# Performance work log

Measured on AMD Instinct MI355X. Metric: run time of the kernel, lower is better.

Reference implementation:

```python
import jax, jax.numpy as jnp
import numpy as np

B, S, D, H, HD = 4, 2048, 1024, 16, 64
MLP = 4 * D
ROPE_BASE = 10000.0
TARGET_SPARSITY = 0.2


def _rotate_half(t):
    return jnp.concatenate([-t[..., HD // 2:], t[..., :HD // 2]], axis=-1)


def setup_inputs() -> dict:
    key = jax.random.key(0)
    ks = jax.random.split(key, 10)
    s = 0.02
    return {
        "x": jax.random.normal(ks[0], (B, S, D), jnp.float32),
        "gate_w": jax.random.normal(ks[1], (D, 1), jnp.float32) * s,
        "gate_b": jnp.zeros((1,), jnp.float32),
        "wq": jax.random.normal(ks[2], (D, D), jnp.float32) * s,
        "wk": jax.random.normal(ks[3], (D, D), jnp.float32) * s,
        "wv": jax.random.normal(ks[4], (D, D), jnp.float32) * s,
        "wo": jax.random.normal(ks[5], (D, D), jnp.float32) * s,
        "conv_w": jax.random.normal(ks[6], (D, 3), jnp.float32) * s,  # depthwise k=3
        "conv_b": jnp.zeros((D,), jnp.float32),
        "mlp_w1": jax.random.normal(ks[7], (D, MLP), jnp.float32) * s,
        "mlp_b1": jnp.zeros((MLP,), jnp.float32),
        "mlp_w2": jax.random.normal(ks[8], (MLP, D), jnp.float32) * s,
        "mlp_b2": jnp.zeros((D,), jnp.float32),
    }


def reference(x, gate_w, gate_b, wq, wk, wv, wo, conv_w, conv_b,
              mlp_w1, mlp_b1, mlp_w2, mlp_b2):
    # --- Router (eval path: hard threshold, mask_ste == active mask) ---
    logits = x @ gate_w + gate_b                    # [B,S,1]
    probs = jax.nn.sigmoid(logits)
    aux_loss = (probs.mean() - TARGET_SPARSITY) ** 2
    mask = (probs > 0.5).astype(x.dtype)            # [B,S,1]

    # --- Reflexive stream: causal depthwise conv (left pad 2) + MLP ---
    xp = jnp.pad(x, ((0, 0), (2, 0), (0, 0)))       # [B,S+2,D]
    x_conv = (xp[:, 0:S] * conv_w[:, 0]
              + xp[:, 1:S + 1] * conv_w[:, 1]
              + xp[:, 2:S + 2] * conv_w[:, 2] + conv_b)
    shallow = jax.nn.relu(x_conv @ mlp_w1 + mlp_b1) @ mlp_w2 + mlp_b2

    # --- Contextual stream: RoPE causal attention, queries gated by router ---
    q = (x @ wq).reshape(B, S, H, HD)
    k = (x @ wk).reshape(B, S, H, HD)
    v = (x @ wv).reshape(B, S, H, HD)

    pos = jnp.arange(S)
    inv_freq = 1.0 / (ROPE_BASE ** (jnp.arange(0, HD, 2, dtype=jnp.float32) / HD))
    freqs = pos[:, None].astype(jnp.float32) * inv_freq[None, :]
    emb = jnp.concatenate([freqs, freqs], axis=-1)  # [S,HD]
    cos = jnp.cos(emb)[None, :, None, :]
    sin = jnp.sin(emb)[None, :, None, :]
    q = q * cos + _rotate_half(q) * sin
    k = k * cos + _rotate_half(k) * sin

    scale = 1.0 / np.sqrt(HD)
    scores = jnp.einsum('bqhd,bkhd->bhqk', q, k) * scale
    causal = pos[:, None] >= pos[None, :]           # [S,S]
    scores = jnp.where(causal[None, None], scores, jnp.finfo(scores.dtype).min)
    attn = jax.nn.softmax(scores, axis=-1)
    ctx = jnp.einsum('bhqk,bkhd->bqhd', attn, v).reshape(B, S, D)
    ctx = (ctx @ wo) * mask                         # scatter back: only active queries contribute

    out = x + shallow + ctx
    return out, aux_loss
```

## Files before the change

### kernel.cpp

```cpp
#include <hip/hip_runtime.h>
#include <hip/hip_bf16.h>

#define DDIM 1024
#define SLEN 2048
#define NTOK 8192
#define MLPD 4096

typedef float f32x4 __attribute__((ext_vector_type(4)));
typedef __bf16 bf16x8 __attribute__((ext_vector_type(8)));

__device__ __forceinline__ void async16(void* lds, const void* g) {
  __builtin_amdgcn_global_load_lds(
      (__attribute__((address_space(1))) void*)g,
      (__attribute__((address_space(3))) void*)lds, 16, 0, 0);
}

template <int N> struct VMC { static constexpr int v = N; };

__global__ __launch_bounds__(256) void prep_kernel(
    const float* __restrict__ x, const float* __restrict__ gate_w,
    const float* __restrict__ gate_b, const float* __restrict__ conv_w,
    const float* __restrict__ conv_b, __bf16* __restrict__ xb,
    __bf16* __restrict__ xcb, float* __restrict__ maskp,
    float* __restrict__ probsp) {
  const int tok = blockIdx.x, t = threadIdx.x;
  const int s = tok & (SLEN - 1);
  const float* xr = x + (size_t)tok * DDIM;
  float4 v = ((const float4*)xr)[t];
  float4 g = ((const float4*)gate_w)[t];
  float part = v.x * g.x + v.y * g.y + v.z * g.z + v.w * g.w;
#pragma unroll
  for (int d = 32; d; d >>= 1) part += __shfl_down(part, d);
  __shared__ float ws4[4];
  const int lane = t & 63, w = t >> 6;
  if (lane == 0) ws4[w] = part;
  __syncthreads();
  if (t == 0) {
    float logit = ws4[0] + ws4[1] + ws4[2] + ws4[3] + gate_b[0];
    float prob = 1.f / (1.f + __expf(-logit));
    probsp[tok] = prob;
    maskp[tok] = prob > 0.5f ? 1.f : 0.f;
  }
  union { ushort4 u; __bf16 b[4]; } xo;
  xo.b[0] = (__bf16)v.x; xo.b[1] = (__bf16)v.y;
  xo.b[2] = (__bf16)v.z; xo.b[3] = (__bf16)v.w;
  ((ushort4*)(xb + (size_t)tok * DDIM))[t] = xo.u;
  float4 zero4 = {0.f, 0.f, 0.f, 0.f};
  float4 m1 = (s >= 1) ? ((const float4*)(xr - DDIM))[t] : zero4;
  float4 m2 = (s >= 2) ? ((const float4*)(xr - 2 * DDIM))[t] : zero4;
  int d0 = t * 4;
  float vv[4] = {v.x, v.y, v.z, v.w};
  float a1[4] = {m1.x, m1.y, m1.z, m1.w};
  float a2[4] = {m2.x, m2.y, m2.z, m2.w};
  union { ushort4 u; __bf16 b[4]; } co;
#pragma unroll
  for (int i = 0; i < 4; ++i) {
    float c0 = conv_w[(d0 + i) * 3 + 0];
    float c1 = conv_w[(d0 + i) * 3 + 1];
    float c2 = conv_w[(d0 + i) * 3 + 2];
    float r = a2[i] * c0 + a1[i] * c1 + vv[i] * c2 + conv_b[d0 + i];
    co.b[i] = (__bf16)r;
  }
  ((ushort4*)(xcb + (size_t)tok * DDIM))[t] = co.u;
}

__global__ __launch_bounds__(256) void tabgen_kernel(float2* __restrict__ tab) {
  const int idx = blockIdx.x * 256 + threadIdx.x;
  const int s = idx >> 5, i = idx & 31;
  float invf = __builtin_amdgcn_exp2f(-(float)i * (13.28771238f / 32.f));
  float fr = (float)s * invf;
  tab[idx] = make_float2(cosf(fr), sinf(fr));
}

__global__ __launch_bounds__(256) void tcast_kernel(const float* __restrict__ src,
                                                    __bf16* __restrict__ dst,
                                                    int K, int N) {
  __shared__ __bf16 tile[64][65];
  const int n0 = blockIdx.x * 64, k0 = blockIdx.y * 64;
  const int t = threadIdx.x;
  const int cr = (t & 15) * 4;
#pragma unroll
  for (int i = 0; i < 4; ++i) {
    int rr = (t >> 4) + i * 16;
    float4 v = *(const float4*)(src + (size_t)(k0 + rr) * N + n0 + cr);
    tile[rr][cr + 0] = (__bf16)v.x; tile[rr][cr + 1] = (__bf16)v.y;
    tile[rr][cr + 2] = (__bf16)v.z; tile[rr][cr + 3] = (__bf16)v.w;
  }
  __syncthreads();
#pragma unroll
  for (int i = 0; i < 2; ++i) {
    int c = t + i * 256;
    int nl = c >> 3, koff = (c & 7) * 8;
    union { uint4 u; __bf16 b[8]; } o;
#pragma unroll
    for (int j = 0; j < 8; ++j) o.b[j] = tile[koff + j][nl];
    *(uint4*)(dst + (size_t)(n0 + nl) * K + k0 + koff) = o.u;
  }
}

template <int EPI, bool ROPE>
__global__ __launch_bounds__(512, 2) void gemm256p(
    const __bf16* __restrict__ A, const __bf16* __restrict__ Bt,
    const float* __restrict__ bias, const float2* __restrict__ tab,
    __bf16* __restrict__ Cb, int M, int N, int K) {
  extern __shared__ char sm[];
  const int t = threadIdx.x, lane = t & 63, w = t >> 6;
  const int c = lane & 15, g = lane >> 4;
  const int nwg = gridDim.x * gridDim.y;
  const int wgid = blockIdx.y * gridDim.x + blockIdx.x;
  const int swz = (wgid & 7) * (nwg >> 3) + (wgid >> 3);
  const int m0 = (swz / gridDim.x) * 256, n0 = (swz % gridDim.x) * 256;
  const int wm = (w >> 2) * 128, wn = (w & 3) * 64;

  f32x4 acc[8][4] = {};
  const int nk = K >> 5;

  auto stage = [&](int buf, int kt) {
    const int k0 = kt << 5;
    char* base = sm + buf * 32768;
#pragma unroll
    for (int r = 0; r < 2; ++r) {
      int o = ((r * 8 + w) << 10) + (lane << 4);
      int rp = o >> 7;
      int u = (o >> 4) & 7;
      int l = u ^ (rp & 7);
      int mr = rp * 2 + (l >> 2);
      int kk = (l & 3) * 8;
      async16(base + o, A + (size_t)(m0 + mr) * K + k0 + kk);
      async16(base + 16384 + o, Bt + (size_t)(n0 + mr) * K + k0 + kk);
    }
  };

  auto body = [&](auto vmc, int tt, bool dostage) {
    if (dostage) stage((tt + 3) & 3, tt + 3);
    asm volatile("s_waitcnt vmcnt(%0)" ::"n"(decltype(vmc)::v) : "memory");
    __builtin_amdgcn_s_barrier();
    asm volatile("" ::: "memory");
    const char* Ab = sm + (tt & 3) * 32768;
    const char* Bb = Ab + 16384;
    bf16x8 aq[8], bq[4];
#pragma unroll
    for (int nt = 0; nt < 4; ++nt) {
      int row = wn + nt * 16 + c;
      int rp = row >> 1;
      int u = ((row & 1) * 4 + g) ^ (rp & 7);
      bq[nt] = *(const bf16x8*)(Bb + rp * 128 + u * 16);
    }
#pragma unroll
    for (int i = 0; i < 8; ++i) {
      int row = wm + i * 16 + c;
      int rp = row >> 1;
      int u = ((row & 1) * 4 + g) ^ (rp & 7);
      aq[i] = *(const bf16x8*)(Ab + rp * 128 + u * 16);
    }
    __builtin_amdgcn_s_setprio(1);
#pragma unroll
    for (int i = 0; i < 8; ++i)
#pragma unroll
      for (int nt = 0; nt < 4; ++nt)
        acc[i][nt] = __builtin_amdgcn_mfma_f32_16x16x32_bf16(
            aq[i], bq[nt], acc[i][nt], 0, 0, 0);
    __builtin_amdgcn_s_setprio(0);
    __builtin_amdgcn_s_barrier();
    asm volatile("" ::: "memory");
  };

  stage(0, 0);
  stage(1, 1);
  stage(2, 2);
  int tt = 0;
  for (; tt < nk - 3; ++tt) body(VMC<12>{}, tt, true);
  body(VMC<8>{}, tt, false); ++tt;
  body(VMC<4>{}, tt, false); ++tt;
  body(VMC<0>{}, tt, false);

  if (ROPE && n0 < 2048) {
#pragma unroll
    for (int i = 0; i < 8; ++i)
#pragma unroll
      for (int r = 0; r < 4; ++r) {
        int s = (m0 + wm + i * 16 + g * 4 + r) & (SLEN - 1);
        float2 t0 = tab[s * 32 + c];
        float2 t1 = tab[s * 32 + 16 + c];
        float q0 = acc[i][0][r], q2 = acc[i][2][r];
        acc[i][0][r] = q0 * t0.x - q2 * t0.y;
        acc[i][2][r] = q2 * t0.x + q0 * t0.y;
        float q1 = acc[i][1][r], q3 = acc[i][3][r];
        acc[i][1][r] = q1 * t1.x - q3 * t1.y;
        acc[i][3][r] = q3 * t1.x + q1 * t1.y;
      }
  }

#pragma unroll
  for (int i = 0; i < 8; ++i)
#pragma unroll
    for (int nt = 0; nt < 4; ++nt)
#pragma unroll
      for (int r = 0; r < 4; ++r) {
        int row = m0 + wm + i * 16 + g * 4 + r;
        int col = n0 + wn + nt * 16 + c;
        float v = acc[i][nt][r];
        size_t idx = (size_t)row * N + col;
        if constexpr (EPI == 0) {
          Cb[idx] = (__bf16)v;
        } else {
          v += bias[col];
          Cb[idx] = (__bf16)fmaxf(v, 0.f);
        }
      }
}

template <int EPI>
__global__ __launch_bounds__(256, 3) void gemm_bt(
    const __bf16* __restrict__ A, const __bf16* __restrict__ Bt,
    const float* __restrict__ bias, const float* __restrict__ xres,
    const float* __restrict__ maskp, __bf16* __restrict__ Cb,
    float* __restrict__ Cf, int M, int N, int K) {
  __shared__ char smem[32768];
  char* As = smem;
  char* Bs = smem + 16384;
  const int t = threadIdx.x, lane = t & 63, w = t >> 6;
  const int nwg = gridDim.x * gridDim.y;
  const int wgid = blockIdx.y * gridDim.x + blockIdx.x;
  const int swz = (wgid & 7) * (nwg >> 3) + (wgid >> 3);
  const int m0 = (swz / gridDim.x) * 128, n0 = (swz % gridDim.x) * 128;
  const int wm = (w >> 1) * 64, wn = (w & 1) * 64;
  f32x4 acc[4][4] = {};
  const int nk = K >> 6;
  for (int kt = 0; kt < nk; ++kt) {
    const int k0 = kt << 6;
#pragma unroll
    for (int rd = 0; rd < 4; ++rd) {
      int o = ((rd * 4 + w) << 10) + (lane << 4);
      int row = o >> 7;
      int us = ((o >> 4) & 7) ^ (row & 7);
      async16(As + o, A + (size_t)(m0 + row) * K + k0 + us * 8);
      async16(Bs + o, Bt + (size_t)(n0 + row) * K + k0 + us * 8);
    }
    __syncthreads();
#pragma unroll
    for (int ks = 0; ks < 2; ++ks) {
      bf16x8 af[4], bfr[4];
#pragma unroll
      for (int mt = 0; mt < 4; ++mt) {
        int row = wm + mt * 16 + (lane & 15);
        int u = (ks * 4 + (lane >> 4)) ^ (row & 7);
        af[mt] = *(const bf16x8*)(As + row * 128 + u * 16);
      }
#pragma unroll
      for (int nt = 0; nt < 4; ++nt) {
        int row = wn + nt * 16 + (lane & 15);
        int u = (ks * 4 + (lane >> 4)) ^ (row & 7);
        bfr[nt] = *(const bf16x8*)(Bs + row * 128 + u * 16);
      }
#pragma unroll
      for (int mt = 0; mt < 4; ++mt)
#pragma unroll
        for (int nt = 0; nt < 4; ++nt)
          acc[mt][nt] = __builtin_amdgcn_mfma_f32_16x16x32_bf16(
              af[mt], bfr[nt], acc[mt][nt], 0, 0, 0);
    }
    __syncthreads();
  }
#pragma unroll
  for (int mt = 0; mt < 4; ++mt)
#pragma unroll
    for (int nt = 0; nt < 4; ++nt)
#pragma unroll
      for (int r = 0; r < 4; ++r) {
        int row = m0 + wm + mt * 16 + ((lane >> 4) << 2) + r;
        int col = n0 + wn + nt * 16 + (lane & 15);
        float v = acc[mt][nt][r];
        size_t idx = (size_t)row * N + col;
        if constexpr (EPI == 2) {
          Cf[idx] = xres[idx] + v + bias[col];
        } else {
          Cf[idx] += maskp[row] * v;
        }
      }
}

__device__ __forceinline__ void scatterV(char* Vdst, int w, int lane,
                                         float4 va, float4 vb) {
  union { float4 f; __bf16 bv[8]; } u0, u1;
  u0.f = va; u1.f = vb;
#pragma unroll
  for (int j = 0; j < 8; ++j) {
    int d = w * 8 + j;
    int by = d * 128 + (((lane >> 3) ^ (d & 7)) << 4) + ((lane & 7) << 1);
    *(__bf16*)(Vdst + by) = u0.bv[j];
    int d2 = d + 32;
    int by2 = d2 * 128 + (((lane >> 3) ^ (d2 & 7)) << 4) + ((lane & 7) << 1);
    *(__bf16*)(Vdst + by2) = u1.bv[j];
  }
}

__global__ __launch_bounds__(256, 3) void attn_kernel(const __bf16* __restrict__ qkv,
                                                      __bf16* __restrict__ ctx) {
  __shared__ char sm[32768];
  const int t = threadIdx.x, lane = t & 63, w = t >> 6;
  const int c = lane & 15, g = lane >> 4, g4 = g * 4;
  const int bh = (int)blockIdx.x * 8 + ((int)blockIdx.y & 7);
  const int qp = (int)blockIdx.y >> 3;
  const int h = bh & 15, b = bh >> 4;
  const size_t tokbase = (size_t)b * SLEN;
  const __bf16* qg = qkv + tokbase * 3072 + h * 64;
  const __bf16* kg = qg + 1024;
  const __bf16* vg = qg + 2048;
  const float SCL = 0.125f * 1.44269504f;
  char* Ps = sm + (w << 12);
  char* Ks = sm + 16384;
  char* Vs = sm + 24576;

  for (int ph = 0; ph < 2; ++ph) {
    const int qt = ph == 0 ? qp : 15 - qp;
    const int q0 = qt * 128;
#pragma unroll
    for (int rd = 0; rd < 4; ++rd) {
      int o = ((rd * 4 + w) << 10) + (lane << 4);
      int row = o >> 7;
      int us = ((o >> 4) & 7) ^ (row & 7);
      async16(sm + o, qg + (size_t)(q0 + row) * 3072 + us * 8);
    }
    __syncthreads();
    bf16x8 qb[2][2];
#pragma unroll
    for (int mt = 0; mt < 2; ++mt)
#pragma unroll
      for (int ks = 0; ks < 2; ++ks) {
        int row = w * 32 + mt * 16 + c;
        int u = (ks * 4 + g) ^ (row & 7);
        qb[mt][ks] = *(const bf16x8*)(sm + row * 128 + u * 16);
      }

    float m_run[2] = {-1e30f, -1e30f}, l_run[2] = {0.f, 0.f};
    f32x4 o_acc[2][4] = {};
    const int nkt = (q0 + 128) >> 6;
    const int wrow0 = q0 + w * 32;

    for (int kt = 0; kt < nkt; ++kt) {
      const int k0 = kt << 6;
#pragma unroll
      for (int rd = 0; rd < 2; ++rd) {
        int o = ((rd * 4 + w) << 10) + (lane << 4);
        int row = o >> 7;
        int us = ((o >> 4) & 7) ^ (row & 7);
        async16(Ks + o, kg + (size_t)(k0 + row) * 3072 + us * 8);
      }
      {
        float4 va = *(const float4*)(vg + (size_t)(k0 + lane) * 3072 + w * 8);
        float4 vb2 = *(const float4*)(vg + (size_t)(k0 + lane) * 3072 + w * 8 + 32);
        scatterV(Vs, w, lane, va, vb2);
      }
      __syncthreads();
      if (k0 <= wrow0 + 31) {
        f32x4 st[4][2] = {};
        __builtin_amdgcn_s_setprio(1);
#pragma unroll
        for (int ks = 0; ks < 2; ++ks) {
          bf16x8 ka[4];
#pragma unroll
          for (int nt = 0; nt < 4; ++nt) {
            int row = nt * 16 + c;
            int u = (ks * 4 + g) ^ (row & 7);
            ka[nt] = *(const bf16x8*)(Ks + row * 128 + u * 16);
          }
#pragma unroll
          for (int nt = 0; nt < 4; ++nt)
#pragma unroll
            for (int mt = 0; mt < 2; ++mt)
              st[nt][mt] = __builtin_amdgcn_mfma_f32_16x16x32_bf16(
                  ka[nt], qb[mt][ks], st[nt][mt], 0, 0, 0);
        }
        __builtin_amdgcn_s_setprio(0);
        const bool needmask = (k0 + 63) > wrow0;
#pragma unroll
        for (int mt = 0; mt < 2; ++mt) {
          float mx = -1e30f;
          if (needmask) {
            int qglob = wrow0 + mt * 16 + c;
#pragma unroll
            for (int nt = 0; nt < 4; ++nt)
#pragma unroll
              for (int r = 0; r < 4; ++r) {
                float sv = st[nt][mt][r] * SCL;
                if (k0 + nt * 16 + g4 + r > qglob) sv = -1e30f;
                st[nt][mt][r] = sv;
                mx = fmaxf(mx, sv);
              }
          } else {
#pragma unroll
            for (int nt = 0; nt < 4; ++nt)
#pragma unroll
              for (int r = 0; r < 4; ++r) {
                float sv = st[nt][mt][r] * SCL;
                st[nt][mt][r] = sv;
                mx = fmaxf(mx, sv);
              }
          }
          mx = fmaxf(mx, __shfl_xor(mx, 16));
          mx = fmaxf(mx, __shfl_xor(mx, 32));
          const bool skip = __all(mx - m_run[mt] <= 8.f) != 0;
          float mnew = skip ? m_run[mt] : fmaxf(m_run[mt], mx);
          float rs = 0.f;
#pragma unroll
          for (int nt = 0; nt < 4; ++nt)
#pragma unroll
            for (int r = 0; r < 4; ++r) {
              float p = __builtin_amdgcn_exp2f(st[nt][mt][r] - mnew);
              st[nt][mt][r] = p;
              rs += p;
            }
          rs += __shfl_xor(rs, 16);
          rs += __shfl_xor(rs, 32);
          if (skip) {
            l_run[mt] += rs;
          } else {
            float fac = __builtin_amdgcn_exp2f(m_run[mt] - mnew);
            m_run[mt] = mnew;
            l_run[mt] = l_run[mt] * fac + rs;
#pragma unroll
            for (int r = 0; r < 4; ++r) {
              float fr = __shfl(fac, g * 20 + r);
#pragma unroll
              for (int dt = 0; dt < 4; ++dt) o_acc[mt][dt][r] *= fr;
            }
          }
          int rowq = mt * 16 + c;
          int rbase = rowq * 128 + 8 * (g & 1);
#pragma unroll
          for (int nt = 0; nt < 4; ++nt) {
            int us = (2 * nt + (g >> 1)) ^ (c & 7);
            union { uint2 v; __bf16 bb[4]; } pp;
            pp.bb[0] = (__bf16)st[nt][mt][0]; pp.bb[1] = (__bf16)st[nt][mt][1];
            pp.bb[2] = (__bf16)st[nt][mt][2]; pp.bb[3] = (__bf16)st[nt][mt][3];
            *(uint2*)(Ps + rbase + us * 16) = pp.v;
          }
        }
        __builtin_amdgcn_s_setprio(1);
#pragma unroll
        for (int ks = 0; ks < 2; ++ks) {
          bf16x8 pa[2], vb[4];
#pragma unroll
          for (int mt = 0; mt < 2; ++mt) {
            int row = mt * 16 + c;
            int u = (ks * 4 + g) ^ (row & 7);
            pa[mt] = *(const bf16x8*)(Ps + row * 128 + u * 16);
          }
#pragma unroll
          for (int dt = 0; dt < 4; ++dt) {
            int row = dt * 16 + c;
            int u = (ks * 4 + g) ^ (row & 7);
            vb[dt] = *(const bf16x8*)(Vs + row * 128 + u * 16);
          }
#pragma unroll
          for (int mt = 0; mt < 2; ++mt)
#pragma unroll
            for (int dt = 0; dt < 4; ++dt)
              o_acc[mt][dt] = __builtin_amdgcn_mfma_f32_16x16x32_bf16(
                  pa[mt], vb[dt], o_acc[mt][dt], 0, 0, 0);
        }
        __builtin_amdgcn_s_setprio(0);
      }
      __syncthreads();
    }
#pragma unroll
    for (int mt = 0; mt < 2; ++mt)
#pragma unroll
      for (int r = 0; r < 4; ++r) {
        float lr = __shfl(l_run[mt], g * 20 + r);
        float inv = 1.f / lr;
        int tokr = q0 + w * 32 + mt * 16 + g4 + r;
#pragma unroll
        for (int dt = 0; dt < 4; ++dt) {
          int d = dt * 16 + c;
          ctx[(tokbase + tokr) * DDIM + h * 64 + d] =
              (__bf16)(o_acc[mt][dt][r] * inv);
        }
      }
  }
}

__global__ __launch_bounds__(256) void aux_kernel(const float* __restrict__ probsp,
                                                  float* __restrict__ outp) {
  const int t = threadIdx.x;
  float sum = 0.f;
  for (int i = t; i < NTOK; i += 256) sum += probsp[i];
#pragma unroll
  for (int d = 32; d; d >>= 1) sum += __shfl_down(sum, d);
  __shared__ float ws4[4];
  if ((t & 63) == 0) ws4[t >> 6] = sum;
  __syncthreads();
  if (t == 0) {
    float m = (ws4[0] + ws4[1] + ws4[2] + ws4[3]) * (1.f / NTOK) - 0.2f;
    outp[0] = m * m;
  }
}

extern "C" void kernel_launch(void* const* d_in, const int* in_sizes, int n_in,
                              void* d_out, int out_size, void* d_ws, size_t ws_size,
                              hipStream_t stream) {
  const float* x      = (const float*)d_in[0];
  const float* gate_w = (const float*)d_in[1];
  const float* gate_b = (const float*)d_in[2];
  const float* wq     = (const float*)d_in[3];
  const float* wk     = (const float*)d_in[4];
  const float* wv     = (const float*)d_in[5];
  const float* wo     = (const float*)d_in[6];
  const float* conv_w = (const float*)d_in[7];
  const float* conv_b = (const float*)d_in[8];
  const float* mlp_w1 = (const float*)d_in[9];
  const float* mlp_b1 = (const float*)d_in[10];
  const float* mlp_w2 = (const float*)d_in[11];
  const float* mlp_b2 = (const float*)d_in[12];
  float* out = (float*)d_out;

  char* ws = (char*)d_ws;
  const size_t MB = 1ull << 20;
  __bf16* xb     = (__bf16*)(ws + 0);
  __bf16* xcb    = (__bf16*)(ws + 16 * MB);
  __bf16* ctx    = (__bf16*)(ws + 16 * MB);
  __bf16* wqkv_t = (__bf16*)(ws + 32 * MB);
  __bf16* wo_t   = (__bf16*)(ws + 38 * MB);
  __bf16* w1_t   = (__bf16*)(ws + 40 * MB);
  __bf16* w2_t   = (__bf16*)(ws + 48 * MB);
  float*  maskp  = (float*)(ws + 56 * MB);
  float*  probsp = (float*)(ws + 56 * MB + 65536);
  float2* ropetab= (float2*)(ws + 56 * MB + 131072);
  __bf16* h1     = (__bf16*)(ws + 57 * MB);
  __bf16* qkv    = (__bf16*)(ws + 57 * MB);

  prep_kernel<<<NTOK, 256, 0, stream>>>(x, gate_w, gate_b, conv_w, conv_b,
                                        xb, xcb, maskp, probsp);
  tabgen_kernel<<<256, 256, 0, stream>>>(ropetab);
  tcast_kernel<<<dim3(16, 16), 256, 0, stream>>>(wq, wqkv_t, 1024, 1024);
  tcast_kernel<<<dim3(16, 16), 256, 0, stream>>>(wk, wqkv_t + 1024 * 1024, 1024, 1024);
  tcast_kernel<<<dim3(16, 16), 256, 0, stream>>>(wv, wqkv_t + 2048 * 1024, 1024, 1024);
  tcast_kernel<<<dim3(16, 16), 256, 0, stream>>>(wo, wo_t, 1024, 1024);
  tcast_kernel<<<dim3(64, 16), 256, 0, stream>>>(mlp_w1, w1_t, 1024, 4096);
  tcast_kernel<<<dim3(16, 64), 256, 0, stream>>>(mlp_w2, w2_t, 4096, 1024);

  gemm256p<1, false><<<dim3(16, 32), 512, 131072, stream>>>(
      xcb, w1_t, mlp_b1, nullptr, h1, NTOK, MLPD, DDIM);
  gemm_bt<2><<<dim3(8, 64), 256, 0, stream>>>(h1, w2_t, mlp_b2, x, nullptr,
                                              nullptr, out, NTOK, DDIM, MLPD);
  gemm256p<0, true><<<dim3(12, 32), 512, 131072, stream>>>(
      xb, wqkv_t, nullptr, ropetab, qkv, NTOK, 3072, DDIM);
  attn_kernel<<<dim3(8, 64), 256, 0, stream>>>(qkv, ctx);
  gemm_bt<3><<<dim3(8, 64), 256, 0, stream>>>(ctx, wo_t, nullptr, nullptr, maskp,
                                              nullptr, out, NTOK, DDIM, DDIM);
  aux_kernel<<<1, 256, 0, stream>>>(probsp, out + (size_t)(out_size - 1));
}
```

Measured before the change: 393.4 us.

## Compact router-active queries and skip inactive tokens in attention and Wo GEMM

Adds a compaction kernel that builds a per-batch list of tokens whose router mask is active. Attention loads only those query rows through the index list, limits each tile's key range to the largest active position, and writes compacted context. The Wo GEMM skips row tiles beyond the active count and scatter-adds results to the original token rows, which removes the mask multiply. This cuts attention and output-projection work in proportion to sparsity. In exchange it adds a serial scan kernel, gather indirection, and load imbalance across attention blocks.

```diff
diff --git a/kernel.cpp b/kernel.cpp
--- a/kernel.cpp
+++ b/kernel.cpp
@@ -62,6 +62,35 @@
     co.b[i] = (__bf16)r;
   }
   ((ushort4*)(xcb + (size_t)tok * DDIM))[t] = co.u;
+}
+
+__global__ __launch_bounds__(256) void compact_kernel(
+    const float* __restrict__ maskp, int* __restrict__ act,
+    int* __restrict__ nact) {
+  const int b = blockIdx.x, t = threadIdx.x;
+  __shared__ int sc[256];
+  __shared__ int base;
+  if (t == 0) base = 0;
+  __syncthreads();
+  for (int ch = 0; ch < 8; ++ch) {
+    int tok = ch * 256 + t;
+    int m = maskp[b * 2048 + tok] > 0.5f ? 1 : 0;
+    sc[t] = m;
+    __syncthreads();
+#pragma unroll
+    for (int off = 1; off < 256; off <<= 1) {
+      int v = t >= off ? sc[t - off] : 0;
+      __syncthreads();
+      sc[t] += v;
+      __syncthreads();
+    }
+    if (m) act[b * 2048 + base + sc[t] - 1] = tok;
+    int tot = sc[255];
+    __syncthreads();
+    if (t == 0) base += tot;
+    __syncthreads();
+  }
+  if (t == 0) nact[b] = base;
 }
 
 __global__ __launch_bounds__(256) void tabgen_kernel(float2* __restrict__ tab) {
@@ -210,11 +239,9 @@
       }
 }
 
-template <int EPI>
-__global__ __launch_bounds__(256, 3) void gemm_bt(
+__global__ __launch_bounds__(256, 3) void gemm_bt2(
     const __bf16* __restrict__ A, const __bf16* __restrict__ Bt,
     const float* __restrict__ bias, const float* __restrict__ xres,
-    const float* __restrict__ maskp, __bf16* __restrict__ Cb,
     float* __restrict__ Cf, int M, int N, int K) {
   __shared__ char smem[32768];
   char* As = smem;
@@ -270,12 +297,76 @@
       for (int r = 0; r < 4; ++r) {
         int row = m0 + wm + mt * 16 + ((lane >> 4) << 2) + r;
         int col = n0 + wn + nt * 16 + (lane & 15);
-        float v = acc[mt][nt][r];
         size_t idx = (size_t)row * N + col;
-        if constexpr (EPI == 2) {
-          Cf[idx] = xres[idx] + v + bias[col];
-        } else {
-          Cf[idx] += maskp[row] * v;
+        Cf[idx] = xres[idx] + acc[mt][nt][r] + bias[col];
+      }
+}
+
+__global__ __launch_bounds__(256, 3) void gemm_wo(
+    const __bf16* __restrict__ A, const __bf16* __restrict__ Bt,
+    const int* __restrict__ act, const int* __restrict__ nact,
+    float* __restrict__ Cf, int M, int N, int K) {
+  __shared__ char smem[32768];
+  char* As = smem;
+  char* Bs = smem + 16384;
+  const int t = threadIdx.x, lane = t & 63, w = t >> 6;
+  const int nwg = gridDim.x * gridDim.y;
+  const int wgid = blockIdx.y * gridDim.x + blockIdx.x;
+  const int swz = (wgid & 7) * (nwg >> 3) + (wgid >> 3);
+  const int m0 = (swz / gridDim.x) * 128, n0 = (swz % gridDim.x) * 128;
+  const int b = m0 >> 11;
+  const int na = nact[b];
+  if ((m0 & 2047) >= na) return;
+  const int wm = (w >> 1) * 64, wn = (w & 1) * 64;
+  f32x4 acc[4][4] = {};
+  const int nk = K >> 6;
+  for (int kt = 0; kt < nk; ++kt) {
+    const int k0 = kt << 6;
+#pragma unroll
+    for (int rd = 0; rd < 4; ++rd) {
+      int o = ((rd * 4 + w) << 10) + (lane << 4);
+      int row = o >> 7;
+      int us = ((o >> 4) & 7) ^ (row & 7);
+      async16(As + o, A + (size_t)(m0 + row) * K + k0 + us * 8);
+      async16(Bs + o, Bt + (size_t)(n0 + row) * K + k0 + us * 8);
+    }
+    __syncthreads();
+#pragma unroll
+    for (int ks = 0; ks < 2; ++ks) {
+      bf16x8 af[4], bfr[4];
+#pragma unroll
+      for (int mt = 0; mt < 4; ++mt) {
+        int row = wm + mt * 16 + (lane & 15);
+        int u = (ks * 4 + (lane >> 4)) ^ (row & 7);
+        af[mt] = *(const bf16x8*)(As + row * 128 + u * 16);
+      }
+#pragma unroll
+      for (int nt = 0; nt < 4; ++nt) {
+        int row = wn + nt * 16 + (lane & 15);
+        int u = (ks * 4 + (lane >> 4)) ^ (row & 7);
+        bfr[nt] = *(const bf16x8*)(Bs + row * 128 + u * 16);
+      }
+#pragma unroll
+      for (int mt = 0; mt < 4; ++mt)
+#pragma unroll
+        for (int nt = 0; nt < 4; ++nt)
+          acc[mt][nt] = __builtin_amdgcn_mfma_f32_16x16x32_bf16(
+              af[mt], bfr[nt], acc[mt][nt], 0, 0, 0);
+    }
+    __syncthreads();
+  }
+#pragma unroll
+  for (int mt = 0; mt < 4; ++mt)
+#pragma unroll
+    for (int nt = 0; nt < 4; ++nt)
+#pragma unroll
+      for (int r = 0; r < 4; ++r) {
+        int row = m0 + wm + mt * 16 + ((lane >> 4) << 2) + r;
+        int col = n0 + wn + nt * 16 + (lane & 15);
+        int jj = row & 2047;
+        if (jj < na) {
+          int tok = act[b * 2048 + jj];
+          Cf[((size_t)b * 2048 + tok) * N + col] += acc[mt][nt][r];
         }
       }
 }
@@ -295,14 +386,19 @@
   }
 }
 
-__global__ __launch_bounds__(256, 3) void attn_kernel(const __bf16* __restrict__ qkv,
-                                                      __bf16* __restrict__ ctx) {
+__global__ __launch_bounds__(256, 3) void attn_kernel(
+    const __bf16* __restrict__ qkv, __bf16* __restrict__ ctx,
+    const int* __restrict__ act, const int* __restrict__ nact) {
   __shared__ char sm[32768];
   const int t = threadIdx.x, lane = t & 63, w = t >> 6;
   const int c = lane & 15, g = lane >> 4, g4 = g * 4;
-  const int bh = (int)blockIdx.x * 8 + ((int)blockIdx.y & 7);
-  const int qp = (int)blockIdx.y >> 3;
+  const int bh = (int)blockIdx.x;
   const int h = bh & 15, b = bh >> 4;
+  const int na = nact[b];
+  const int ntile = (na + 127) >> 7;
+  const int j = 15 - (int)blockIdx.y;
+  if (j >= ntile) return;
+  const int* actb = act + b * 2048;
   const size_t tokbase = (size_t)b * SLEN;
   const __bf16* qg = qkv + tokbase * 3072 + h * 64;
   const __bf16* kg = qg + 1024;
@@ -312,173 +408,180 @@
   char* Ks = sm + 16384;
   char* Vs = sm + 24576;
 
-  for (int ph = 0; ph < 2; ++ph) {
-    const int qt = ph == 0 ? qp : 15 - qp;
-    const int q0 = qt * 128;
-#pragma unroll
-    for (int rd = 0; rd < 4; ++rd) {
+  const int q0 = j * 128;
+#pragma unroll
+  for (int rd = 0; rd < 4; ++rd) {
+    int o = ((rd * 4 + w) << 10) + (lane << 4);
+    int row = o >> 7;
+    int us = ((o >> 4) & 7) ^ (row & 7);
+    int cr = q0 + row; if (cr > na - 1) cr = na - 1;
+    async16(sm + o, qg + (size_t)actb[cr] * 3072 + us * 8);
+  }
+  __syncthreads();
+  bf16x8 qb[2][2];
+#pragma unroll
+  for (int mt = 0; mt < 2; ++mt)
+#pragma unroll
+    for (int ks = 0; ks < 2; ++ks) {
+      int row = w * 32 + mt * 16 + c;
+      int u = (ks * 4 + g) ^ (row & 7);
+      qb[mt][ks] = *(const bf16x8*)(sm + row * 128 + u * 16);
+    }
+  int qpos[2];
+#pragma unroll
+  for (int mt = 0; mt < 2; ++mt) {
+    int rr = q0 + w * 32 + mt * 16 + c; if (rr > na - 1) rr = na - 1;
+    qpos[mt] = actb[rr];
+  }
+  int rf = q0 + w * 32;       if (rf > na - 1) rf = na - 1;
+  int rl = q0 + w * 32 + 31;  if (rl > na - 1) rl = na - 1;
+  const int wmin = actb[rf], wmax = actb[rl];
+  int bl = q0 + 127;          if (bl > na - 1) bl = na - 1;
+  const int nkt = (actb[bl] >> 6) + 1;
+
+  float m_run[2] = {-1e30f, -1e30f}, l_run[2] = {0.f, 0.f};
+  f32x4 o_acc[2][4] = {};
+
+  for (int kt = 0; kt < nkt; ++kt) {
+    const int k0 = kt << 6;
+#pragma unroll
+    for (int rd = 0; rd < 2; ++rd) {
       int o = ((rd * 4 + w) << 10) + (lane << 4);
       int row = o >> 7;
       int us = ((o >> 4) & 7) ^ (row & 7);
-      async16(sm + o, qg + (size_t)(q0 + row) * 3072 + us * 8);
-    }
-    __syncthreads();
-    bf16x8 qb[2][2];
-#pragma unroll
-    for (int mt = 0; mt < 2; ++mt)
+      async16(Ks + o, kg + (size_t)(k0 + row) * 3072 + us * 8);
+    }
+    {
+      float4 va = *(const float4*)(vg + (size_t)(k0 + lane) * 3072 + w * 8);
+      float4 vb2 = *(const float4*)(vg + (size_t)(k0 + lane) * 3072 + w * 8 + 32);
+      scatterV(Vs, w, lane, va, vb2);
+    }
+    __syncthreads();
+    if (k0 <= wmax) {
+      f32x4 st[4][2] = {};
+      __builtin_amdgcn_s_setprio(1);
 #pragma unroll
       for (int ks = 0; ks < 2; ++ks) {
-        int row = w * 32 + mt * 16 + c;
-        int u = (ks * 4 + g) ^ (row & 7);
-        qb[mt][ks] = *(const bf16x8*)(sm + row * 128 + u * 16);
-      }
-
-    float m_run[2] = {-1e30f, -1e30f}, l_run[2] = {0.f, 0.f};
-    f32x4 o_acc[2][4] = {};
-    const int nkt = (q0 + 128) >> 6;
-    const int wrow0 = q0 + w * 32;
-
-    for (int kt = 0; kt < nkt; ++kt) {
-      const int k0 = kt << 6;
-#pragma unroll
-      for (int rd = 0; rd < 2; ++rd) {
-        int o = ((rd * 4 + w) << 10) + (lane << 4);
-        int row = o >> 7;
-        int us = ((o >> 4) & 7) ^ (row & 7);
-        async16(Ks + o, kg + (size_t)(k0 + row) * 3072 + us * 8);
-      }
-      {
-        float4 va = *(const float4*)(vg + (size_t)(k0 + lane) * 3072 + w * 8);
-        float4 vb2 = *(const float4*)(vg + (size_t)(k0 + lane) * 3072 + w * 8 + 32);
-        scatterV(Vs, w, lane, va, vb2);
-      }
-      __syncthreads();
-      if (k0 <= wrow0 + 31) {
-        f32x4 st[4][2] = {};
-        __builtin_amdgcn_s_setprio(1);
-#pragma unroll
-        for (int ks = 0; ks < 2; ++ks) {
-          bf16x8 ka[4];
-#pragma unroll
-          for (int nt = 0; nt < 4; ++nt) {
-            int row = nt * 16 + c;
-            int u = (ks * 4 + g) ^ (row & 7);
-            ka[nt] = *(const bf16x8*)(Ks + row * 128 + u * 16);
+        bf16x8 ka[4];
+#pragma unroll
+        for (int nt = 0; nt < 4; ++nt) {
+          int row = nt * 16 + c;
+          int u = (ks * 4 + g) ^ (row & 7);
+          ka[nt] = *(const bf16x8*)(Ks + row * 128 + u * 16);
+        }
+#pragma unroll
+        for (int nt = 0; nt < 4; ++nt)
+#pragma unroll
+          for (int mt = 0; mt < 2; ++mt)
+            st[nt][mt] = __builtin_amdgcn_mfma_f32_16x16x32_bf16(
+                ka[nt], qb[mt][ks], st[nt][mt], 0, 0, 0);
+      }
+      __builtin_amdgcn_s_setprio(0);
+      const bool needmask = (k0 + 63) > wmin;
+#pragma unroll
+      for (int mt = 0; mt < 2; ++mt) {
+        float mx = -1e30f;
+        if (needmask) {
+          int qglob = qpos[mt];
+#pragma unroll
+          for (int nt = 0; nt < 4; ++nt)
+#pragma unroll
+            for (int r = 0; r < 4; ++r) {
+              float sv = st[nt][mt][r] * SCL;
+              if (k0 + nt * 16 + g4 + r > qglob) sv = -1e30f;
+              st[nt][mt][r] = sv;
+              mx = fmaxf(mx, sv);
+            }
+        } else {
+#pragma unroll
+          for (int nt = 0; nt < 4; ++nt)
+#pragma unroll
+            for (int r = 0; r < 4; ++r) {
+              float sv = st[nt][mt][r] * SCL;
+              st[nt][mt][r] = sv;
+              mx = fmaxf(mx, sv);
+            }
+        }
+        mx = fmaxf(mx, __shfl_xor(mx, 16));
+        mx = fmaxf(mx, __shfl_xor(mx, 32));
+        const bool skip = __all(mx - m_run[mt] <= 8.f) != 0;
+        float mnew = skip ? m_run[mt] : fmaxf(m_run[mt], mx);
+        float rs = 0.f;
+#pragma unroll
+        for (int nt = 0; nt < 4; ++nt)
+#pragma unroll
+          for (int r = 0; r < 4; ++r) {
+            float p = __builtin_amdgcn_exp2f(st[nt][mt][r] - mnew);
+            st[nt][mt][r] = p;
+            rs += p;
           }
-#pragma unroll
-          for (int nt = 0; nt < 4; ++nt)
-#pragma unroll
-            for (int mt = 0; mt < 2; ++mt)
-              st[nt][mt] = __builtin_amdgcn_mfma_f32_16x16x32_bf16(
-                  ka[nt], qb[mt][ks], st[nt][mt], 0, 0, 0);
-        }
-        __builtin_amdgcn_s_setprio(0);
-        const bool needmask = (k0 + 63) > wrow0;
+        rs += __shfl_xor(rs, 16);
+        rs += __shfl_xor(rs, 32);
+        if (skip) {
+          l_run[mt] += rs;
+        } else {
+          float fac = __builtin_amdgcn_exp2f(m_run[mt] - mnew);
+          m_run[mt] = mnew;
+          l_run[mt] = l_run[mt] * fac + rs;
+#pragma unroll
+          for (int r = 0; r < 4; ++r) {
+            float fr = __shfl(fac, g * 20 + r);
+#pragma unroll
+            for (int dt = 0; dt < 4; ++dt) o_acc[mt][dt][r] *= fr;
+          }
+        }
+        int rowq = mt * 16 + c;
+        int rbase = rowq * 128 + 8 * (g & 1);
+#pragma unroll
+        for (int nt = 0; nt < 4; ++nt) {
+          int us = (2 * nt + (g >> 1)) ^ (c & 7);
+          union { uint2 v; __bf16 bb[4]; } pp;
+          pp.bb[0] = (__bf16)st[nt][mt][0]; pp.bb[1] = (__bf16)st[nt][mt][1];
+          pp.bb[2] = (__bf16)st[nt][mt][2]; pp.bb[3] = (__bf16)st[nt][mt][3];
+          *(uint2*)(Ps + rbase + us * 16) = pp.v;
+        }
+      }
+      __builtin_amdgcn_s_setprio(1);
+#pragma unroll
+      for (int ks = 0; ks < 2; ++ks) {
+        bf16x8 pa[2], vb[4];
 #pragma unroll
         for (int mt = 0; mt < 2; ++mt) {
-          float mx = -1e30f;
-          if (needmask) {
-            int qglob = wrow0 + mt * 16 + c;
-#pragma unroll
-            for (int nt = 0; nt < 4; ++nt)
-#pragma unroll
-              for (int r = 0; r < 4; ++r) {
-                float sv = st[nt][mt][r] * SCL;
-                if (k0 + nt * 16 + g4 + r > qglob) sv = -1e30f;
-                st[nt][mt][r] = sv;
-                mx = fmaxf(mx, sv);
-              }
-          } else {
-#pragma unroll
-            for (int nt = 0; nt < 4; ++nt)
-#pragma unroll
-              for (int r = 0; r < 4; ++r) {
-                float sv = st[nt][mt][r] * SCL;
-                st[nt][mt][r] = sv;
-                mx = fmaxf(mx, sv);
-              }
-          }
-          mx = fmaxf(mx, __shfl_xor(mx, 16));
-          mx = fmaxf(mx, __shfl_xor(mx, 32));
-          const bool skip = __all(mx - m_run[mt] <= 8.f) != 0;
-          float mnew = skip ? m_run[mt] : fmaxf(m_run[mt], mx);
-          float rs = 0.f;
-#pragma unroll
-          for (int nt = 0; nt < 4; ++nt)
-#pragma unroll
-            for (int r = 0; r < 4; ++r) {
-              float p = __builtin_amdgcn_exp2f(st[nt][mt][r] - mnew);
-              st[nt][mt][r] = p;
-              rs += p;
-            }
-          rs += __shfl_xor(rs, 16);
-          rs += __shfl_xor(rs, 32);
-          if (skip) {
-            l_run[mt] += rs;
-          } else {
-            float fac = __builtin_amdgcn_exp2f(m_run[mt] - mnew);
-            m_run[mt] = mnew;
-            l_run[mt] = l_run[mt] * fac + rs;
-#pragma unroll
-            for (int r = 0; r < 4; ++r) {
-              float fr = __shfl(fac, g * 20 + r);
-#pragma unroll
-              for (int dt = 0; dt < 4; ++dt) o_acc[mt][dt][r] *= fr;
-            }
-          }
-          int rowq = mt * 16 + c;
-          int rbase = rowq * 128 + 8 * (g & 1);
-#pragma unroll
-          for (int nt = 0; nt < 4; ++nt) {
-            int us = (2 * nt + (g >> 1)) ^ (c & 7);
-            union { uint2 v; __bf16 bb[4]; } pp;
-            pp.bb[0] = (__bf16)st[nt][mt][0]; pp.bb[1] = (__bf16)st[nt][mt][1];
-            pp.bb[2] = (__bf16)st[nt][mt][2]; pp.bb[3] = (__bf16)st[nt][mt][3];
-            *(uint2*)(Ps + rbase + us * 16) = pp.v;
-          }
-        }
-        __builtin_amdgcn_s_setprio(1);
-#pragma unroll
-        for (int ks = 0; ks < 2; ++ks) {
-          bf16x8 pa[2], vb[4];
-#pragma unroll
-          for (int mt = 0; mt < 2; ++mt) {
-            int row = mt * 16 + c;
-            int u = (ks * 4 + g) ^ (row & 7);
-            pa[mt] = *(const bf16x8*)(Ps + row * 128 + u * 16);
-          }
-#pragma unroll
-          for (int dt = 0; dt < 4; ++dt) {
-            int row = dt * 16 + c;
-            int u = (ks * 4 + g) ^ (row & 7);
-            vb[dt] = *(const bf16x8*)(Vs + row * 128 + u * 16);
-          }
-#pragma unroll
-          for (int mt = 0; mt < 2; ++mt)
-#pragma unroll
-            for (int dt = 0; dt < 4; ++dt)
-              o_acc[mt][dt] = __builtin_amdgcn_mfma_f32_16x16x32_bf16(
-                  pa[mt], vb[dt], o_acc[mt][dt], 0, 0, 0);
-        }
-        __builtin_amdgcn_s_setprio(0);
-      }
-      __syncthreads();
-    }
-#pragma unroll
-    for (int mt = 0; mt < 2; ++mt)
-#pragma unroll
-      for (int r = 0; r < 4; ++r) {
-        float lr = __shfl(l_run[mt], g * 20 + r);
-        float inv = 1.f / lr;
-        int tokr = q0 + w * 32 + mt * 16 + g4 + r;
+          int row = mt * 16 + c;
+          int u = (ks * 4 + g) ^ (row & 7);
+          pa[mt] = *(const bf16x8*)(Ps + row * 128 + u * 16);
+        }
 #pragma unroll
         for (int dt = 0; dt < 4; ++dt) {
-          int d = dt * 16 + c;
-          ctx[(tokbase + tokr) * DDIM + h * 64 + d] =
-              (__bf16)(o_acc[mt][dt][r] * inv);
-        }
-      }
-  }
+          int row = dt * 16 + c;
+          int u = (ks * 4 + g) ^ (row & 7);
+          vb[dt] = *(const bf16x8*)(Vs + row * 128 + u * 16);
+        }
+#pragma unroll
+        for (int mt = 0; mt < 2; ++mt)
+#pragma unroll
+          for (int dt = 0; dt < 4; ++dt)
+            o_acc[mt][dt] = __builtin_amdgcn_mfma_f32_16x16x32_bf16(
+                pa[mt], vb[dt], o_acc[mt][dt], 0, 0, 0);
+      }
+      __builtin_amdgcn_s_setprio(0);
+    }
+    __syncthreads();
+  }
+#pragma unroll
+  for (int mt = 0; mt < 2; ++mt)
+#pragma unroll
+    for (int r = 0; r < 4; ++r) {
+      float lr = __shfl(l_run[mt], g * 20 + r);
+      float inv = 1.f / lr;
+      int tokr = q0 + w * 32 + mt * 16 + g4 + r;
+#pragma unroll
+      for (int dt = 0; dt < 4; ++dt) {
+        int d = dt * 16 + c;
+        ctx[(tokbase + tokr) * DDIM + h * 64 + d] =
+            (__bf16)(o_acc[mt][dt][r] * inv);
+      }
+    }
 }
 
 __global__ __launch_bounds__(256) void aux_kernel(const float* __restrict__ probsp,
@@ -527,11 +630,14 @@
   float*  maskp  = (float*)(ws + 56 * MB);
   float*  probsp = (float*)(ws + 56 * MB + 65536);
   float2* ropetab= (float2*)(ws + 56 * MB + 131072);
+  int*    act    = (int*)(ws + 56 * MB + 655360);
+  int*    nactp  = (int*)(ws + 56 * MB + 688128);
   __bf16* h1     = (__bf16*)(ws + 57 * MB);
   __bf16* qkv    = (__bf16*)(ws + 57 * MB);
 
   prep_kernel<<<NTOK, 256, 0, stream>>>(x, gate_w, gate_b, conv_w, conv_b,
                                         xb, xcb, maskp, probsp);
+  compact_kernel<<<4, 256, 0, stream>>>(maskp, act, nactp);
   tabgen_kernel<<<256, 256, 0, stream>>>(ropetab);
   tcast_kernel<<<dim3(16, 16), 256, 0, stream>>>(wq, wqkv_t, 1024, 1024);
   tcast_kernel<<<dim3(16, 16), 256, 0, stream>>>(wk, wqkv_t + 1024 * 1024, 1024, 1024);
@@ -542,12 +648,12 @@
 
   gemm256p<1, false><<<dim3(16, 32), 512, 131072, stream>>>(
       xcb, w1_t, mlp_b1, nullptr, h1, NTOK, MLPD, DDIM);
-  gemm_bt<2><<<dim3(8, 64), 256, 0, stream>>>(h1, w2_t, mlp_b2, x, nullptr,
-                                              nullptr, out, NTOK, DDIM, MLPD);
+  gemm_bt2<<<dim3(8, 64), 256, 0, stream>>>(h1, w2_t, mlp_b2, x, out,
+                                            NTOK, DDIM, MLPD);
   gemm256p<0, true><<<dim3(12, 32), 512, 131072, stream>>>(
       xb, wqkv_t, nullptr, ropetab, qkv, NTOK, 3072, DDIM);
-  attn_kernel<<<dim3(8, 64), 256, 0, stream>>>(qkv, ctx);
-  gemm_bt<3><<<dim3(8, 64), 256, 0, stream>>>(ctx, wo_t, nullptr, nullptr, maskp,
-                                              nullptr, out, NTOK, DDIM, DDIM);
+  attn_kernel<<<dim3(64, 16), 256, 0, stream>>>(qkv, ctx, act, nactp);
+  gemm_wo<<<dim3(8, 64), 256, 0, stream>>>(ctx, wo_t, act, nactp, out,
+                                           NTOK, DDIM, DDIM);
   aux_kernel<<<1, 256, 0, stream>>>(probsp, out + (size_t)(out_size - 1));
 }
```

After: 412.7 us. +4.9%, slower.

## Split attention work across 8 waves of 16 query rows and batch weight casts

Applied to the files above, without the earlier changes.

The attention kernel now runs 512 threads per block, with each of the 8 waves owning 16 query rows instead of 32. K/V tile loading is split across twice as many waves, and the per-wave P buffer shrinks to fit in the same LDS. This is meant to raise occupancy and latency hiding, at the cost of fewer MFMAs per K/V LDS read and more barrier participants. The four 1024x1024 weight transpose-casts are also merged into one launch to cut launch overhead.

```diff
diff --git a/kernel.cpp b/kernel.cpp
--- a/kernel.cpp
+++ b/kernel.cpp
@@ -72,11 +72,10 @@
   tab[idx] = make_float2(cosf(fr), sinf(fr));
 }
 
-__global__ __launch_bounds__(256) void tcast_kernel(const float* __restrict__ src,
-                                                    __bf16* __restrict__ dst,
-                                                    int K, int N) {
+__device__ __forceinline__ void tcast_body(const float* __restrict__ src,
+                                           __bf16* __restrict__ dst,
+                                           int K, int N, int n0, int k0) {
   __shared__ __bf16 tile[64][65];
-  const int n0 = blockIdx.x * 64, k0 = blockIdx.y * 64;
   const int t = threadIdx.x;
   const int cr = (t & 15) * 4;
 #pragma unroll
@@ -96,6 +95,22 @@
     for (int j = 0; j < 8; ++j) o.b[j] = tile[koff + j][nl];
     *(uint4*)(dst + (size_t)(n0 + nl) * K + k0 + koff) = o.u;
   }
+}
+
+__global__ __launch_bounds__(256) void tcast_kernel(const float* __restrict__ src,
+                                                    __bf16* __restrict__ dst,
+                                                    int K, int N) {
+  tcast_body(src, dst, K, N, blockIdx.x * 64, blockIdx.y * 64);
+}
+
+__global__ __launch_bounds__(256) void tcast4_kernel(
+    const float* __restrict__ s0, const float* __restrict__ s1,
+    const float* __restrict__ s2, const float* __restrict__ s3,
+    __bf16* __restrict__ dqkv, __bf16* __restrict__ dwo) {
+  const int z = blockIdx.z;
+  const float* src = z == 0 ? s0 : z == 1 ? s1 : z == 2 ? s2 : s3;
+  __bf16* dst = z < 3 ? dqkv + (size_t)z * 1024 * 1024 : dwo;
+  tcast_body(src, dst, 1024, 1024, blockIdx.x * 64, blockIdx.y * 64);
 }
 
 template <int EPI, bool ROPE>
@@ -280,22 +295,18 @@
       }
 }
 
-__device__ __forceinline__ void scatterV(char* Vdst, int w, int lane,
-                                         float4 va, float4 vb) {
-  union { float4 f; __bf16 bv[8]; } u0, u1;
-  u0.f = va; u1.f = vb;
+__device__ __forceinline__ void scatterV8(char* Vdst, int w, int lane, float4 va) {
+  union { float4 f; __bf16 bv[8]; } u0;
+  u0.f = va;
 #pragma unroll
   for (int j = 0; j < 8; ++j) {
     int d = w * 8 + j;
     int by = d * 128 + (((lane >> 3) ^ (d & 7)) << 4) + ((lane & 7) << 1);
     *(__bf16*)(Vdst + by) = u0.bv[j];
-    int d2 = d + 32;
-    int by2 = d2 * 128 + (((lane >> 3) ^ (d2 & 7)) << 4) + ((lane & 7) << 1);
-    *(__bf16*)(Vdst + by2) = u1.bv[j];
-  }
-}
-
-__global__ __launch_bounds__(256, 3) void attn_kernel(const __bf16* __restrict__ qkv,
+  }
+}
+
+__global__ __launch_bounds__(512, 4) void attn_kernel(const __bf16* __restrict__ qkv,
                                                       __bf16* __restrict__ ctx) {
   __shared__ char sm[32768];
   const int t = threadIdx.x, lane = t & 63, w = t >> 6;
@@ -308,7 +319,7 @@
   const __bf16* kg = qg + 1024;
   const __bf16* vg = qg + 2048;
   const float SCL = 0.125f * 1.44269504f;
-  char* Ps = sm + (w << 12);
+  char* Ps = sm + (w << 11);
   char* Ks = sm + 16384;
   char* Vs = sm + 24576;
 
@@ -316,45 +327,39 @@
     const int qt = ph == 0 ? qp : 15 - qp;
     const int q0 = qt * 128;
 #pragma unroll
-    for (int rd = 0; rd < 4; ++rd) {
-      int o = ((rd * 4 + w) << 10) + (lane << 4);
+    for (int rd = 0; rd < 2; ++rd) {
+      int o = ((rd * 8 + w) << 10) + (lane << 4);
       int row = o >> 7;
       int us = ((o >> 4) & 7) ^ (row & 7);
       async16(sm + o, qg + (size_t)(q0 + row) * 3072 + us * 8);
     }
     __syncthreads();
-    bf16x8 qb[2][2];
-#pragma unroll
-    for (int mt = 0; mt < 2; ++mt)
-#pragma unroll
-      for (int ks = 0; ks < 2; ++ks) {
-        int row = w * 32 + mt * 16 + c;
-        int u = (ks * 4 + g) ^ (row & 7);
-        qb[mt][ks] = *(const bf16x8*)(sm + row * 128 + u * 16);
-      }
-
-    float m_run[2] = {-1e30f, -1e30f}, l_run[2] = {0.f, 0.f};
-    f32x4 o_acc[2][4] = {};
+    bf16x8 qb[2];
+#pragma unroll
+    for (int ks = 0; ks < 2; ++ks) {
+      int row = w * 16 + c;
+      int u = (ks * 4 + g) ^ (row & 7);
+      qb[ks] = *(const bf16x8*)(sm + row * 128 + u * 16);
+    }
+
+    float m_run = -1e30f, l_run = 0.f;
+    f32x4 o_acc[4] = {};
     const int nkt = (q0 + 128) >> 6;
-    const int wrow0 = q0 + w * 32;
+    const int wrow0 = q0 + w * 16;
 
     for (int kt = 0; kt < nkt; ++kt) {
       const int k0 = kt << 6;
-#pragma unroll
-      for (int rd = 0; rd < 2; ++rd) {
-        int o = ((rd * 4 + w) << 10) + (lane << 4);
+      {
+        int o = (w << 10) + (lane << 4);
         int row = o >> 7;
         int us = ((o >> 4) & 7) ^ (row & 7);
         async16(Ks + o, kg + (size_t)(k0 + row) * 3072 + us * 8);
-      }
-      {
         float4 va = *(const float4*)(vg + (size_t)(k0 + lane) * 3072 + w * 8);
-        float4 vb2 = *(const float4*)(vg + (size_t)(k0 + lane) * 3072 + w * 8 + 32);
-        scatterV(Vs, w, lane, va, vb2);
+        scatterV8(Vs, w, lane, va);
       }
       __syncthreads();
-      if (k0 <= wrow0 + 31) {
-        f32x4 st[4][2] = {};
+      if (k0 <= wrow0 + 15) {
+        f32x4 st[4] = {};
         __builtin_amdgcn_s_setprio(1);
 #pragma unroll
         for (int ks = 0; ks < 2; ++ks) {
@@ -367,85 +372,79 @@
           }
 #pragma unroll
           for (int nt = 0; nt < 4; ++nt)
-#pragma unroll
-            for (int mt = 0; mt < 2; ++mt)
-              st[nt][mt] = __builtin_amdgcn_mfma_f32_16x16x32_bf16(
-                  ka[nt], qb[mt][ks], st[nt][mt], 0, 0, 0);
+            st[nt] = __builtin_amdgcn_mfma_f32_16x16x32_bf16(
+                ka[nt], qb[ks], st[nt], 0, 0, 0);
         }
         __builtin_amdgcn_s_setprio(0);
         const bool needmask = (k0 + 63) > wrow0;
-#pragma unroll
-        for (int mt = 0; mt < 2; ++mt) {
-          float mx = -1e30f;
-          if (needmask) {
-            int qglob = wrow0 + mt * 16 + c;
-#pragma unroll
-            for (int nt = 0; nt < 4; ++nt)
-#pragma unroll
-              for (int r = 0; r < 4; ++r) {
-                float sv = st[nt][mt][r] * SCL;
-                if (k0 + nt * 16 + g4 + r > qglob) sv = -1e30f;
-                st[nt][mt][r] = sv;
-                mx = fmaxf(mx, sv);
-              }
-          } else {
-#pragma unroll
-            for (int nt = 0; nt < 4; ++nt)
-#pragma unroll
-              for (int r = 0; r < 4; ++r) {
-                float sv = st[nt][mt][r] * SCL;
-                st[nt][mt][r] = sv;
-                mx = fmaxf(mx, sv);
-              }
+        float mx = -1e30f;
+        if (needmask) {
+          int qglob = wrow0 + c;
+#pragma unroll
+          for (int nt = 0; nt < 4; ++nt)
+#pragma unroll
+            for (int r = 0; r < 4; ++r) {
+              float sv = st[nt][r] * SCL;
+              if (k0 + nt * 16 + g4 + r > qglob) sv = -1e30f;
+              st[nt][r] = sv;
+              mx = fmaxf(mx, sv);
+            }
+        } else {
+#pragma unroll
+          for (int nt = 0; nt < 4; ++nt)
+#pragma unroll
+            for (int r = 0; r < 4; ++r) {
+              float sv = st[nt][r] * SCL;
+              st[nt][r] = sv;
+              mx = fmaxf(mx, sv);
+            }
+        }
+        mx = fmaxf(mx, __shfl_xor(mx, 16));
+        mx = fmaxf(mx, __shfl_xor(mx, 32));
+        const bool skip = __all(mx - m_run <= 8.f) != 0;
+        float mnew = skip ? m_run : fmaxf(m_run, mx);
+        float rs = 0.f;
+#pragma unroll
+        for (int nt = 0; nt < 4; ++nt)
+#pragma unroll
+          for (int r = 0; r < 4; ++r) {
+            float p = __builtin_amdgcn_exp2f(st[nt][r] - mnew);
+            st[nt][r] = p;
+            rs += p;
           }
-          mx = fmaxf(mx, __shfl_xor(mx, 16));
-          mx = fmaxf(mx, __shfl_xor(mx, 32));
-          const bool skip = __all(mx - m_run[mt] <= 8.f) != 0;
-          float mnew = skip ? m_run[mt] : fmaxf(m_run[mt], mx);
-          float rs = 0.f;
-#pragma unroll
-          for (int nt = 0; nt < 4; ++nt)
-#pragma unroll
-            for (int r = 0; r < 4; ++r) {
-              float p = __builtin_amdgcn_exp2f(st[nt][mt][r] - mnew);
-              st[nt][mt][r] = p;
-              rs += p;
-            }
-          rs += __shfl_xor(rs, 16);
-          rs += __shfl_xor(rs, 32);
-          if (skip) {
-            l_run[mt] += rs;
-          } else {
-            float fac = __builtin_amdgcn_exp2f(m_run[mt] - mnew);
-            m_run[mt] = mnew;
-            l_run[mt] = l_run[mt] * fac + rs;
-#pragma unroll
-            for (int r = 0; r < 4; ++r) {
-              float fr = __shfl(fac, g * 20 + r);
-#pragma unroll
-              for (int dt = 0; dt < 4; ++dt) o_acc[mt][dt][r] *= fr;
-            }
+        rs += __shfl_xor(rs, 16);
+        rs += __shfl_xor(rs, 32);
+        if (skip) {
+          l_run += rs;
+        } else {
+          float fac = __builtin_amdgcn_exp2f(m_run - mnew);
+          m_run = mnew;
+          l_run = l_run * fac + rs;
+#pragma unroll
+          for (int r = 0; r < 4; ++r) {
+            float fr = __shfl(fac, g * 20 + r);
+#pragma unroll
+            for (int dt = 0; dt < 4; ++dt) o_acc[dt][r] *= fr;
           }
-          int rowq = mt * 16 + c;
-          int rbase = rowq * 128 + 8 * (g & 1);
+        }
+        {
+          int rbase = c * 128 + 8 * (g & 1);
 #pragma unroll
           for (int nt = 0; nt < 4; ++nt) {
             int us = (2 * nt + (g >> 1)) ^ (c & 7);
             union { uint2 v; __bf16 bb[4]; } pp;
-            pp.bb[0] = (__bf16)st[nt][mt][0]; pp.bb[1] = (__bf16)st[nt][mt][1];
-            pp.bb[2] = (__bf16)st[nt][mt][2]; pp.bb[3] = (__bf16)st[nt][mt][3];
+            pp.bb[0] = (__bf16)st[nt][0]; pp.bb[1] = (__bf16)st[nt][1];
+            pp.bb[2] = (__bf16)st[nt][2]; pp.bb[3] = (__bf16)st[nt][3];
             *(uint2*)(Ps + rbase + us * 16) = pp.v;
           }
         }
         __builtin_amdgcn_s_setprio(1);
 #pragma unroll
         for (int ks = 0; ks < 2; ++ks) {
-          bf16x8 pa[2], vb[4];
-#pragma unroll
-          for (int mt = 0; mt < 2; ++mt) {
-            int row = mt * 16 + c;
-            int u = (ks * 4 + g) ^ (row & 7);
-            pa[mt] = *(const bf16x8*)(Ps + row * 128 + u * 16);
+          bf16x8 pa, vb[4];
+          {
+            int u = (ks * 4 + g) ^ (c & 7);
+            pa = *(const bf16x8*)(Ps + c * 128 + u * 16);
           }
 #pragma unroll
           for (int dt = 0; dt < 4; ++dt) {
@@ -454,30 +453,26 @@
             vb[dt] = *(const bf16x8*)(Vs + row * 128 + u * 16);
           }
 #pragma unroll
-          for (int mt = 0; mt < 2; ++mt)
-#pragma unroll
-            for (int dt = 0; dt < 4; ++dt)
-              o_acc[mt][dt] = __builtin_amdgcn_mfma_f32_16x16x32_bf16(
-                  pa[mt], vb[dt], o_acc[mt][dt], 0, 0, 0);
+          for (int dt = 0; dt < 4; ++dt)
+            o_acc[dt] = __builtin_amdgcn_mfma_f32_16x16x32_bf16(
+                pa, vb[dt], o_acc[dt], 0, 0, 0);
         }
         __builtin_amdgcn_s_setprio(0);
       }
       __syncthreads();
     }
 #pragma unroll
-    for (int mt = 0; mt < 2; ++mt)
-#pragma unroll
-      for (int r = 0; r < 4; ++r) {
-        float lr = __shfl(l_run[mt], g * 20 + r);
-        float inv = 1.f / lr;
-        int tokr = q0 + w * 32 + mt * 16 + g4 + r;
-#pragma unroll
-        for (int dt = 0; dt < 4; ++dt) {
-          int d = dt * 16 + c;
-          ctx[(tokbase + tokr) * DDIM + h * 64 + d] =
-              (__bf16)(o_acc[mt][dt][r] * inv);
-        }
-      }
+    for (int r = 0; r < 4; ++r) {
+      float lr = __shfl(l_run, g * 20 + r);
+      float inv = 1.f / lr;
+      int tokr = q0 + w * 16 + g4 + r;
+#pragma unroll
+      for (int dt = 0; dt < 4; ++dt) {
+        int d = dt * 16 + c;
+        ctx[(tokbase + tokr) * DDIM + h * 64 + d] =
+            (__bf16)(o_acc[dt][r] * inv);
+      }
+    }
   }
 }
 
@@ -533,10 +528,8 @@
   prep_kernel<<<NTOK, 256, 0, stream>>>(x, gate_w, gate_b, conv_w, conv_b,
                                         xb, xcb, maskp, probsp);
   tabgen_kernel<<<256, 256, 0, stream>>>(ropetab);
-  tcast_kernel<<<dim3(16, 16), 256, 0, stream>>>(wq, wqkv_t, 1024, 1024);
-  tcast_kernel<<<dim3(16, 16), 256, 0, stream>>>(wk, wqkv_t + 1024 * 1024, 1024, 1024);
-  tcast_kernel<<<dim3(16, 16), 256, 0, stream>>>(wv, wqkv_t + 2048 * 1024, 1024, 1024);
-  tcast_kernel<<<dim3(16, 16), 256, 0, stream>>>(wo, wo_t, 1024, 1024);
+  tcast4_kernel<<<dim3(16, 16, 4), 256, 0, stream>>>(wq, wk, wv, wo,
+                                                     wqkv_t, wo_t);
   tcast_kernel<<<dim3(64, 16), 256, 0, stream>>>(mlp_w1, w1_t, 1024, 4096);
   tcast_kernel<<<dim3(16, 64), 256, 0, stream>>>(mlp_w2, w2_t, 4096, 1024);
 
@@ -546,7 +539,7 @@
                                               nullptr, out, NTOK, DDIM, MLPD);
   gemm256p<0, true><<<dim3(12, 32), 512, 131072, stream>>>(
       xb, wqkv_t, nullptr, ropetab, qkv, NTOK, 3072, DDIM);
-  attn_kernel<<<dim3(8, 64), 256, 0, stream>>>(qkv, ctx);
+  attn_kernel<<<dim3(8, 64), 512, 0, stream>>>(qkv, ctx);
   gemm_bt<3><<<dim3(8, 64), 256, 0, stream>>>(ctx, wo_t, nullptr, nullptr, maskp,
                                               nullptr, out, NTOK, DDIM, DDIM);
   aux_kernel<<<1, 256, 0, stream>>>(probsp, out + (size_t)(out_size - 1));
```

New measurement: 375.6 us. 4.5% less time.
